# Optimization experiments

Measured on AMD Instinct MI355X. Metric: run time of the kernel, lower is better.

Reference implementation:

```python
import jax, jax.numpy as jnp
import numpy as np

N = 100000
E = 1600000
EPS = 1e-5


def gcn_conv(x, W, b, rows, cols, w):
    # x: [N, Fin], rows/cols: [E+N] (self-loops included), w: [E+N]
    h = x @ W  # [N, Fout]
    deg = jax.ops.segment_sum(w, cols, num_segments=N)  # [N]
    dinv = jnp.where(deg > 0, jax.lax.rsqrt(deg), 0.0)
    coef = dinv[rows] * w * dinv[cols]  # [E+N]
    out = jax.ops.segment_sum(coef[:, None] * h[rows], cols, num_segments=N)
    return out + b


def batch_norm(x, g, be):
    mu = jnp.mean(x, axis=0)
    var = jnp.mean(jnp.square(x - mu), axis=0)  # biased, as torch BN
    return (x - mu) * jax.lax.rsqrt(var + EPS) * g + be


def setup_inputs() -> dict:
    key = jax.random.key(0)
    ks = jax.random.split(key, 8)
    x = jax.random.normal(ks[0], (N, 256), dtype=jnp.float32)
    edge_index = jax.random.randint(ks[1], (2, E), 0, N, dtype=jnp.int64)
    edge_weight = jax.random.uniform(ks[2], (E,), dtype=jnp.float32)
    W1 = jax.random.normal(ks[3], (256, 128), dtype=jnp.float32) * (1.0 / np.sqrt(256))
    W2 = jax.random.normal(ks[4], (128, 128), dtype=jnp.float32) * (1.0 / np.sqrt(128))
    W3 = jax.random.normal(ks[5], (128, 64), dtype=jnp.float32) * (1.0 / np.sqrt(128))
    return {
        "x": x, "edge_index": edge_index, "edge_weight": edge_weight,
        "W1": W1, "b1": jnp.zeros(128), "g1": jnp.ones(128), "be1": jnp.zeros(128),
        "W2": W2, "b2": jnp.zeros(128), "g2": jnp.ones(128), "be2": jnp.zeros(128),
        "W3": W3, "b3": jnp.zeros(64),
    }


def reference(x, edge_index, edge_weight, W1, b1, g1, be1, W2, b2, g2, be2, W3, b3):
    # add self-loops (weight 1.0), as PyG GCNConv default
    loops = jnp.arange(N, dtype=edge_index.dtype)
    rows = jnp.concatenate([edge_index[0], loops])
    cols = jnp.concatenate([edge_index[1], loops])
    w = jnp.concatenate([edge_weight, jnp.ones((N,), dtype=edge_weight.dtype)])

    h = gcn_conv(x, W1, b1, rows, cols, w)
    h = jax.nn.relu(batch_norm(h, g1, be1))  # dropout is identity (eval)
    h = gcn_conv(h, W2, b2, rows, cols, w)
    h = jax.nn.relu(batch_norm(h, g2, be2))
    out = gcn_conv(h, W3, b3, rows, cols, w)
    return out
```

## Files before the change

kernel.cpp:

```cpp
#include <hip/hip_runtime.h>
#include <cstddef>


#define WS_ALIGN(x) (((x) + 255) & ~(size_t)255)

__global__ __launch_bounds__(256) void init_kernel(float* deg, int* hist,
                                                   float* sums, float* sumsq,
                                                   int N) {
  int i = blockIdx.x * 256 + threadIdx.x;
  if (i < N) { deg[i] = 1.0f; hist[i] = 0; }
  if (i < 128) { sums[i] = 0.f; sumsq[i] = 0.f; }
}

__global__ __launch_bounds__(256) void edge_deg_kernel(const int* __restrict__ cols,
                                                       const float* __restrict__ w,
                                                       float* __restrict__ deg,
                                                       int* __restrict__ hist, int E) {
  int e = blockIdx.x * 256 + threadIdx.x;
  if (e >= E) return;
  int c = cols[e];
  atomicAdd(&deg[c], w[e]);
  atomicAdd(&hist[c], 1);
}

__global__ __launch_bounds__(256) void dinv_kernel(const float* __restrict__ deg,
                                                   float* __restrict__ dinv, int N) {
  int i = blockIdx.x * 256 + threadIdx.x;
  if (i < N) dinv[i] = rsqrtf(deg[i]);
}

__global__ __launch_bounds__(256) void scan1_kernel(const int* __restrict__ hist,
                                                    int* __restrict__ bsum, int N) {
  int base = blockIdx.x * 2048 + threadIdx.x * 8;
  int s = 0;
#pragma unroll
  for (int j = 0; j < 8; ++j) { int i = base + j; if (i < N) s += hist[i]; }
  __shared__ int ls[256];
  ls[threadIdx.x] = s; __syncthreads();
  for (int st = 128; st > 0; st >>= 1) {
    if (threadIdx.x < st) ls[threadIdx.x] += ls[threadIdx.x + st];
    __syncthreads();
  }
  if (threadIdx.x == 0) bsum[blockIdx.x] = ls[0];
}

__global__ void scan2_kernel(const int* __restrict__ bsum, int* __restrict__ bpref,
                             int nb, int* __restrict__ offsets, int N) {
  if (threadIdx.x == 0) {
    int run = 0;
    for (int b = 0; b < nb; ++b) { bpref[b] = run; run += bsum[b]; }
    offsets[N] = run;
  }
}

__global__ __launch_bounds__(256) void scan3_kernel(const int* __restrict__ hist,
                                                    const int* __restrict__ bpref,
                                                    int* __restrict__ offsets,
                                                    int* __restrict__ cursors, int N) {
  int tid = threadIdx.x;
  int base = blockIdx.x * 2048 + tid * 8;
  int v[8]; int s = 0;
#pragma unroll
  for (int j = 0; j < 8; ++j) { int i = base + j; v[j] = (i < N) ? hist[i] : 0; s += v[j]; }
  __shared__ int ls[256];
  ls[tid] = s; __syncthreads();
  for (int st = 1; st < 256; st <<= 1) {
    int t = (tid >= st) ? ls[tid - st] : 0;
    __syncthreads();
    ls[tid] += t;
    __syncthreads();
  }
  int run = bpref[blockIdx.x] + (ls[tid] - s);
#pragma unroll
  for (int j = 0; j < 8; ++j) {
    int i = base + j;
    if (i < N) { offsets[i] = run; cursors[i] = run; run += v[j]; }
  }
}

__global__ __launch_bounds__(256) void scatter_kernel(const int* __restrict__ rows,
                                                      const int* __restrict__ cols,
                                                      const float* __restrict__ w,
                                                      const float* __restrict__ dinv,
                                                      int* __restrict__ cursors,
                                                      int* __restrict__ srow,
                                                      float* __restrict__ scoef, int E) {
  int e = blockIdx.x * 256 + threadIdx.x;
  if (e >= E) return;
  int r = rows[e], c = cols[e];
  int pos = atomicAdd(&cursors[c], 1);
  srow[pos] = r;
  scoef[pos] = dinv[r] * w[e] * dinv[c];
}

template <int K, int F, int BM, bool PRO>
__global__ __launch_bounds__(256)
void gemm_kernel(const float* __restrict__ A, const float* __restrict__ W,
                 float* __restrict__ out, int M,
                 const float* __restrict__ alpha, const float* __restrict__ beta) {
  constexpr int BK = 32;
  constexpr int TM = 4, TN = 8;
  constexpr int TX = F / TN;
  constexpr int TY = BM / TM;
  static_assert(TX * TY == 256, "bad tile config");
  __shared__ float As[BK][BM];
  __shared__ float Bs[BK][F];
  const int tid = threadIdx.x;
  const int tx = tid % TX;
  const int ty = tid / TX;
  const int row0 = blockIdx.x * BM;
  float acc[TM][TN];
#pragma unroll
  for (int m = 0; m < TM; ++m)
#pragma unroll
    for (int n = 0; n < TN; ++n) acc[m][n] = 0.f;

  const int ar = tid >> 3;
  const int ak = (tid & 7) * 4;

  for (int k0 = 0; k0 < K; k0 += BK) {
#pragma unroll
    for (int p = 0; p < BM / 32; ++p) {
      int r = p * 32 + ar;
      int gr = row0 + r;
      float4 v;
      if (gr < M) v = *(const float4*)(A + (size_t)gr * K + k0 + ak);
      else        v = make_float4(0.f, 0.f, 0.f, 0.f);
      if constexpr (PRO) {
        float4 al = *(const float4*)(alpha + k0 + ak);
        float4 be = *(const float4*)(beta + k0 + ak);
        v.x = fmaxf(fmaf(v.x, al.x, be.x), 0.f);
        v.y = fmaxf(fmaf(v.y, al.y, be.y), 0.f);
        v.z = fmaxf(fmaf(v.z, al.z, be.z), 0.f);
        v.w = fmaxf(fmaf(v.w, al.w, be.w), 0.f);
      }
      As[ak + 0][r] = v.x; As[ak + 1][r] = v.y;
      As[ak + 2][r] = v.z; As[ak + 3][r] = v.w;
    }
#pragma unroll
    for (int p = 0; p < (BK * F) / 1024; ++p) {
      int idx = p * 256 + tid;
      int kk = idx / (F / 4);
      int cc = (idx % (F / 4)) * 4;
      *(float4*)&Bs[kk][cc] = *(const float4*)(W + (size_t)(k0 + kk) * F + cc);
    }
    __syncthreads();
#pragma unroll
    for (int kk = 0; kk < BK; ++kk) {
      float a[TM], b[TN];
      *(float4*)a      = *(const float4*)&As[kk][ty * TM];
      *(float4*)&b[0]  = *(const float4*)&Bs[kk][tx * 4];
      *(float4*)&b[4]  = *(const float4*)&Bs[kk][F / 2 + tx * 4];
#pragma unroll
      for (int m = 0; m < TM; ++m)
#pragma unroll
        for (int n = 0; n < TN; ++n)
          acc[m][n] = fmaf(a[m], b[n], acc[m][n]);
    }
    __syncthreads();
  }
#pragma unroll
  for (int m = 0; m < TM; ++m) {
    int gr = row0 + ty * TM + m;
    if (gr < M) {
      float4* o0 = (float4*)(out + (size_t)gr * F + tx * 4);
      float4* o1 = (float4*)(out + (size_t)gr * F + F / 2 + tx * 4);
      *o0 = make_float4(acc[m][0], acc[m][1], acc[m][2], acc[m][3]);
      *o1 = make_float4(acc[m][4], acc[m][5], acc[m][6], acc[m][7]);
    }
  }
}

template <int F>
__global__ __launch_bounds__(256)
void agg_kernel(const float* __restrict__ h, const int* __restrict__ srow,
                const float* __restrict__ scoef, const int* __restrict__ off,
                const float* __restrict__ dinv, const float* __restrict__ bias,
                float* __restrict__ out, int N) {
  constexpr int VPL = F / 64;
  int wid = blockIdx.x * 4 + (threadIdx.x >> 6);
  if (wid >= N) return;
  int lane = threadIdx.x & 63;
  float d = dinv[wid];
  float acc[VPL];
  {
    const float* hc = h + (size_t)wid * F;
#pragma unroll
    for (int j = 0; j < VPL; ++j)
      acc[j] = d * d * hc[lane * VPL + j] + bias[lane * VPL + j];
  }
  int s = off[wid], e = off[wid + 1];
  int i = s;
  for (; i + 4 <= e; i += 4) {
    int r0 = srow[i], r1 = srow[i + 1], r2 = srow[i + 2], r3 = srow[i + 3];
    float c0 = scoef[i], c1 = scoef[i + 1], c2 = scoef[i + 2], c3 = scoef[i + 3];
    const float* h0 = h + (size_t)r0 * F;
    const float* h1 = h + (size_t)r1 * F;
    const float* h2 = h + (size_t)r2 * F;
    const float* h3 = h + (size_t)r3 * F;
    float v0[VPL], v1[VPL], v2[VPL], v3[VPL];
#pragma unroll
    for (int j = 0; j < VPL; ++j) v0[j] = h0[lane * VPL + j];
#pragma unroll
    for (int j = 0; j < VPL; ++j) v1[j] = h1[lane * VPL + j];
#pragma unroll
    for (int j = 0; j < VPL; ++j) v2[j] = h2[lane * VPL + j];
#pragma unroll
    for (int j = 0; j < VPL; ++j) v3[j] = h3[lane * VPL + j];
#pragma unroll
    for (int j = 0; j < VPL; ++j) acc[j] = fmaf(c0, v0[j], acc[j]);
#pragma unroll
    for (int j = 0; j < VPL; ++j) acc[j] = fmaf(c1, v1[j], acc[j]);
#pragma unroll
    for (int j = 0; j < VPL; ++j) acc[j] = fmaf(c2, v2[j], acc[j]);
#pragma unroll
    for (int j = 0; j < VPL; ++j) acc[j] = fmaf(c3, v3[j], acc[j]);
  }
  for (; i < e; ++i) {
    int r0 = srow[i]; float c0 = scoef[i];
    const float* h0 = h + (size_t)r0 * F;
#pragma unroll
    for (int j = 0; j < VPL; ++j) acc[j] = fmaf(c0, h0[lane * VPL + j], acc[j]);
  }
  float* oc = out + (size_t)wid * F;
#pragma unroll
  for (int j = 0; j < VPL; ++j) oc[lane * VPL + j] = acc[j];
}

__global__ __launch_bounds__(256) void stats_kernel(const float* __restrict__ x, int N,
                                                    float* __restrict__ sums,
                                                    float* __restrict__ sumsq) {
  int f = threadIdx.x & 127;
  int half = threadIdx.x >> 7;
  int rend = min(N, (int)(blockIdx.x + 1) * 64);
  float s = 0.f, ss = 0.f;
  for (int r = blockIdx.x * 64 + half; r < rend; r += 2) {
    float v = x[(size_t)r * 128 + f];
    s += v; ss += v * v;
  }
  __shared__ float ls[256], lss[256];
  ls[threadIdx.x] = s; lss[threadIdx.x] = ss;
  __syncthreads();
  if (half == 0) {
    s += ls[threadIdx.x + 128];
    ss += lss[threadIdx.x + 128];
    atomicAdd(&sums[f], s);
    atomicAdd(&sumsq[f], ss);
  }
}

__global__ void finalize_kernel(const float* __restrict__ g, const float* __restrict__ be,
                                float* __restrict__ sums, float* __restrict__ sumsq,
                                float* __restrict__ alpha, float* __restrict__ beta,
                                float invN) {
  int f = threadIdx.x;
  float mu = sums[f] * invN;
  float var = sumsq[f] * invN - mu * mu;
  float a = g[f] * rsqrtf(var + 1e-5f);
  alpha[f] = a;
  beta[f] = be[f] - mu * a;
  sums[f] = 0.f; sumsq[f] = 0.f;
}

extern "C" void kernel_launch(void* const* d_in, const int* in_sizes, int n_in,
                              void* d_out, int out_size, void* d_ws, size_t ws_size,
                              hipStream_t stream) {
  const float* x   = (const float*)d_in[0];
  const int*   ei  = (const int*)d_in[1];
  const float* ew  = (const float*)d_in[2];
  const float* W1  = (const float*)d_in[3];
  const float* b1  = (const float*)d_in[4];
  const float* g1  = (const float*)d_in[5];
  const float* be1 = (const float*)d_in[6];
  const float* W2  = (const float*)d_in[7];
  const float* b2  = (const float*)d_in[8];
  const float* g2  = (const float*)d_in[9];
  const float* be2 = (const float*)d_in[10];
  const float* W3  = (const float*)d_in[11];
  const float* b3  = (const float*)d_in[12];

  const int N = in_sizes[0] / 256;
  const int E = in_sizes[2];
  const int* rows = ei;
  const int* cols = ei + E;

  char* p = (char*)d_ws;
  auto carve = [&](size_t bytes) { char* q = p; p += WS_ALIGN(bytes); return (void*)q; };
  float* deg     = (float*)carve((size_t)N * 4);
  float* dinv    = (float*)carve((size_t)N * 4);
  int*   hist    = (int*)  carve((size_t)N * 4);
  int*   offsets = (int*)  carve(((size_t)N + 1) * 4);
  int*   cursors = (int*)  carve((size_t)N * 4);
  int*   bsum    = (int*)  carve(256 * 4);
  int*   bpref   = (int*)  carve(256 * 4);
  int*   srow    = (int*)  carve((size_t)E * 4);
  float* scoef   = (float*)carve((size_t)E * 4);
  float* h       = (float*)carve((size_t)N * 128 * 4);
  float* agg     = (float*)carve((size_t)N * 128 * 4);
  float* sums    = (float*)carve(128 * 4);
  float* sumsq   = (float*)carve(128 * 4);
  float* alpha   = (float*)carve(128 * 4);
  float* beta    = (float*)carve(128 * 4);
  (void)ws_size; (void)n_in; (void)out_size;

  const int gN = (N + 255) / 256;
  const int gE = (E + 255) / 256;
  const int nb = (N + 2047) / 2048;

  init_kernel<<<gN, 256, 0, stream>>>(deg, hist, sums, sumsq, N);
  edge_deg_kernel<<<gE, 256, 0, stream>>>(cols, ew, deg, hist, E);
  dinv_kernel<<<gN, 256, 0, stream>>>(deg, dinv, N);
  scan1_kernel<<<nb, 256, 0, stream>>>(hist, bsum, N);
  scan2_kernel<<<1, 64, 0, stream>>>(bsum, bpref, nb, offsets, N);
  scan3_kernel<<<nb, 256, 0, stream>>>(hist, bpref, offsets, cursors, N);
  scatter_kernel<<<gE, 256, 0, stream>>>(rows, cols, ew, dinv, cursors, srow, scoef, E);

  const int gAgg = (N + 3) / 4;

  gemm_kernel<256, 128, 64, false><<<(N + 63) / 64, 256, 0, stream>>>(x, W1, h, N, nullptr, nullptr);
  agg_kernel<128><<<gAgg, 256, 0, stream>>>(h, srow, scoef, offsets, dinv, b1, agg, N);
  stats_kernel<<<(N + 63) / 64, 256, 0, stream>>>(agg, N, sums, sumsq);
  finalize_kernel<<<1, 128, 0, stream>>>(g1, be1, sums, sumsq, alpha, beta, 1.0f / (float)N);

  gemm_kernel<128, 128, 64, true><<<(N + 63) / 64, 256, 0, stream>>>(agg, W2, h, N, alpha, beta);
  agg_kernel<128><<<gAgg, 256, 0, stream>>>(h, srow, scoef, offsets, dinv, b2, agg, N);
  stats_kernel<<<(N + 63) / 64, 256, 0, stream>>>(agg, N, sums, sumsq);
  finalize_kernel<<<1, 128, 0, stream>>>(g2, be2, sums, sumsq, alpha, beta, 1.0f / (float)N);

  gemm_kernel<128, 64, 128, true><<<(N + 127) / 128, 256, 0, stream>>>(agg, W3, h, N, alpha, beta);
  agg_kernel<64><<<gAgg, 256, 0, stream>>>(h, srow, scoef, offsets, dinv, b3, (float*)d_out, N);
}
```

Before: 1.001 ms.

## Pack degree and count into one 64-bit atomic, enlarge GEMM tiles, warp-scan prefix

Edge degree and histogram counting now use a single 64-bit atomic per edge. The weight is stored as 20-bit fixed point in the low bits and the count in the high bits, which halves atomic traffic but makes the degree sum approximate. The block-prefix scan runs as a wavefront shuffle scan instead of a serial loop. The first two GEMMs use 128-row tiles with 8 rows per thread for more register reuse, and As gets a padding column.

```diff
diff --git a/kernel.cpp b/kernel.cpp
--- a/kernel.cpp
+++ b/kernel.cpp
@@ -4,37 +4,41 @@
 
 #define WS_ALIGN(x) (((x) + 255) & ~(size_t)255)
 
-__global__ __launch_bounds__(256) void init_kernel(float* deg, int* hist,
+__global__ __launch_bounds__(256) void init_kernel(unsigned long long* packed,
                                                    float* sums, float* sumsq,
                                                    int N) {
   int i = blockIdx.x * 256 + threadIdx.x;
-  if (i < N) { deg[i] = 1.0f; hist[i] = 0; }
+  if (i < N) packed[i] = 0ull;
   if (i < 128) { sums[i] = 0.f; sumsq[i] = 0.f; }
 }
 
 __global__ __launch_bounds__(256) void edge_deg_kernel(const int* __restrict__ cols,
                                                        const float* __restrict__ w,
-                                                       float* __restrict__ deg,
-                                                       int* __restrict__ hist, int E) {
+                                                       unsigned long long* __restrict__ packed,
+                                                       int E) {
   int e = blockIdx.x * 256 + threadIdx.x;
   if (e >= E) return;
   int c = cols[e];
-  atomicAdd(&deg[c], w[e]);
-  atomicAdd(&hist[c], 1);
-}
-
-__global__ __launch_bounds__(256) void dinv_kernel(const float* __restrict__ deg,
+  unsigned long long v = (1ull << 40) |
+                         (unsigned long long)(unsigned int)__float2uint_rn(w[e] * 1048576.0f);
+  atomicAdd(&packed[c], v);
+}
+
+__global__ __launch_bounds__(256) void dinv_kernel(const unsigned long long* __restrict__ packed,
                                                    float* __restrict__ dinv, int N) {
   int i = blockIdx.x * 256 + threadIdx.x;
-  if (i < N) dinv[i] = rsqrtf(deg[i]);
-}
-
-__global__ __launch_bounds__(256) void scan1_kernel(const int* __restrict__ hist,
+  if (i < N) {
+    float deg = 1.0f + (float)(packed[i] & 0xFFFFFFFFFFull) * (1.0f / 1048576.0f);
+    dinv[i] = rsqrtf(deg);
+  }
+}
+
+__global__ __launch_bounds__(256) void scan1_kernel(const unsigned long long* __restrict__ packed,
                                                     int* __restrict__ bsum, int N) {
   int base = blockIdx.x * 2048 + threadIdx.x * 8;
   int s = 0;
 #pragma unroll
-  for (int j = 0; j < 8; ++j) { int i = base + j; if (i < N) s += hist[i]; }
+  for (int j = 0; j < 8; ++j) { int i = base + j; if (i < N) s += (int)(packed[i] >> 40); }
   __shared__ int ls[256];
   ls[threadIdx.x] = s; __syncthreads();
   for (int st = 128; st > 0; st >>= 1) {
@@ -46,14 +50,18 @@
 
 __global__ void scan2_kernel(const int* __restrict__ bsum, int* __restrict__ bpref,
                              int nb, int* __restrict__ offsets, int N) {
-  if (threadIdx.x == 0) {
-    int run = 0;
-    for (int b = 0; b < nb; ++b) { bpref[b] = run; run += bsum[b]; }
-    offsets[N] = run;
-  }
-}
-
-__global__ __launch_bounds__(256) void scan3_kernel(const int* __restrict__ hist,
+  int lane = threadIdx.x;
+  int mine = (lane < nb) ? bsum[lane] : 0;
+  int v = mine;
+  for (int st = 1; st < 64; st <<= 1) {
+    int t = __shfl_up(v, st, 64);
+    if (lane >= st) v += t;
+  }
+  if (lane < nb) bpref[lane] = v - mine;
+  if (lane == 63) offsets[N] = v;
+}
+
+__global__ __launch_bounds__(256) void scan3_kernel(const unsigned long long* __restrict__ packed,
                                                     const int* __restrict__ bpref,
                                                     int* __restrict__ offsets,
                                                     int* __restrict__ cursors, int N) {
@@ -61,7 +69,11 @@
   int base = blockIdx.x * 2048 + tid * 8;
   int v[8]; int s = 0;
 #pragma unroll
-  for (int j = 0; j < 8; ++j) { int i = base + j; v[j] = (i < N) ? hist[i] : 0; s += v[j]; }
+  for (int j = 0; j < 8; ++j) {
+    int i = base + j;
+    v[j] = (i < N) ? (int)(packed[i] >> 40) : 0;
+    s += v[j];
+  }
   __shared__ int ls[256];
   ls[tid] = s; __syncthreads();
   for (int st = 1; st < 256; st <<= 1) {
@@ -93,17 +105,18 @@
   scoef[pos] = dinv[r] * w[e] * dinv[c];
 }
 
-template <int K, int F, int BM, bool PRO>
+template <int K, int F, int BM, int TM, bool PRO>
 __global__ __launch_bounds__(256)
 void gemm_kernel(const float* __restrict__ A, const float* __restrict__ W,
                  float* __restrict__ out, int M,
                  const float* __restrict__ alpha, const float* __restrict__ beta) {
   constexpr int BK = 32;
-  constexpr int TM = 4, TN = 8;
+  constexpr int TN = 8;
   constexpr int TX = F / TN;
   constexpr int TY = BM / TM;
   static_assert(TX * TY == 256, "bad tile config");
-  __shared__ float As[BK][BM];
+  static_assert(TM == 4 || TM == 8, "TM must be 4 or 8");
+  __shared__ float As[BK][BM + 1];
   __shared__ float Bs[BK][F];
   const int tid = threadIdx.x;
   const int tx = tid % TX;
@@ -148,9 +161,11 @@
 #pragma unroll
     for (int kk = 0; kk < BK; ++kk) {
       float a[TM], b[TN];
-      *(float4*)a      = *(const float4*)&As[kk][ty * TM];
-      *(float4*)&b[0]  = *(const float4*)&Bs[kk][tx * 4];
-      *(float4*)&b[4]  = *(const float4*)&Bs[kk][F / 2 + tx * 4];
+      *(float4*)&a[0] = *(const float4*)&As[kk][ty * 4];
+      if constexpr (TM == 8)
+        *(float4*)&a[4] = *(const float4*)&As[kk][BM / 2 + ty * 4];
+      *(float4*)&b[0] = *(const float4*)&Bs[kk][tx * 4];
+      *(float4*)&b[4] = *(const float4*)&Bs[kk][F / 2 + tx * 4];
 #pragma unroll
       for (int m = 0; m < TM; ++m)
 #pragma unroll
@@ -161,7 +176,7 @@
   }
 #pragma unroll
   for (int m = 0; m < TM; ++m) {
-    int gr = row0 + ty * TM + m;
+    int gr = row0 + ((TM == 8 && m >= 4) ? (BM / 2 + ty * 4 + m - 4) : (ty * 4 + m));
     if (gr < M) {
       float4* o0 = (float4*)(out + (size_t)gr * F + tx * 4);
       float4* o1 = (float4*)(out + (size_t)gr * F + F / 2 + tx * 4);
@@ -286,9 +301,8 @@
 
   char* p = (char*)d_ws;
   auto carve = [&](size_t bytes) { char* q = p; p += WS_ALIGN(bytes); return (void*)q; };
-  float* deg     = (float*)carve((size_t)N * 4);
+  unsigned long long* packed = (unsigned long long*)carve((size_t)N * 8);
   float* dinv    = (float*)carve((size_t)N * 4);
-  int*   hist    = (int*)  carve((size_t)N * 4);
   int*   offsets = (int*)  carve(((size_t)N + 1) * 4);
   int*   cursors = (int*)  carve((size_t)N * 4);
   int*   bsum    = (int*)  carve(256 * 4);
@@ -307,26 +321,27 @@
   const int gE = (E + 255) / 256;
   const int nb = (N + 2047) / 2048;
 
-  init_kernel<<<gN, 256, 0, stream>>>(deg, hist, sums, sumsq, N);
-  edge_deg_kernel<<<gE, 256, 0, stream>>>(cols, ew, deg, hist, E);
-  dinv_kernel<<<gN, 256, 0, stream>>>(deg, dinv, N);
-  scan1_kernel<<<nb, 256, 0, stream>>>(hist, bsum, N);
+  init_kernel<<<gN, 256, 0, stream>>>(packed, sums, sumsq, N);
+  edge_deg_kernel<<<gE, 256, 0, stream>>>(cols, ew, packed, E);
+  dinv_kernel<<<gN, 256, 0, stream>>>(packed, dinv, N);
+  scan1_kernel<<<nb, 256, 0, stream>>>(packed, bsum, N);
   scan2_kernel<<<1, 64, 0, stream>>>(bsum, bpref, nb, offsets, N);
-  scan3_kernel<<<nb, 256, 0, stream>>>(hist, bpref, offsets, cursors, N);
+  scan3_kernel<<<nb, 256, 0, stream>>>(packed, bpref, offsets, cursors, N);
   scatter_kernel<<<gE, 256, 0, stream>>>(rows, cols, ew, dinv, cursors, srow, scoef, E);
 
   const int gAgg = (N + 3) / 4;
-
-  gemm_kernel<256, 128, 64, false><<<(N + 63) / 64, 256, 0, stream>>>(x, W1, h, N, nullptr, nullptr);
+  const int gG = (N + 127) / 128;
+
+  gemm_kernel<256, 128, 128, 8, false><<<gG, 256, 0, stream>>>(x, W1, h, N, nullptr, nullptr);
   agg_kernel<128><<<gAgg, 256, 0, stream>>>(h, srow, scoef, offsets, dinv, b1, agg, N);
   stats_kernel<<<(N + 63) / 64, 256, 0, stream>>>(agg, N, sums, sumsq);
   finalize_kernel<<<1, 128, 0, stream>>>(g1, be1, sums, sumsq, alpha, beta, 1.0f / (float)N);
 
-  gemm_kernel<128, 128, 64, true><<<(N + 63) / 64, 256, 0, stream>>>(agg, W2, h, N, alpha, beta);
+  gemm_kernel<128, 128, 128, 8, true><<<gG, 256, 0, stream>>>(agg, W2, h, N, alpha, beta);
   agg_kernel<128><<<gAgg, 256, 0, stream>>>(h, srow, scoef, offsets, dinv, b2, agg, N);
   stats_kernel<<<(N + 63) / 64, 256, 0, stream>>>(agg, N, sums, sumsq);
   finalize_kernel<<<1, 128, 0, stream>>>(g2, be2, sums, sumsq, alpha, beta, 1.0f / (float)N);
 
-  gemm_kernel<128, 64, 128, true><<<(N + 127) / 128, 256, 0, stream>>>(agg, W3, h, N, alpha, beta);
+  gemm_kernel<128, 64, 128, 4, true><<<gG, 256, 0, stream>>>(agg, W3, h, N, alpha, beta);
   agg_kernel<64><<<gAgg, 256, 0, stream>>>(h, srow, scoef, offsets, dinv, b3, (float*)d_out, N);
 }
```

Measured after the change: 1.079 ms. +7.9%, slower.
